# Kernel tuning notes

Measured on AMD Instinct MI355X. Metric: run time of the kernel, lower is better.

Reference implementation:

```python
import jax, jax.numpy as jnp
import numpy as np

T_STEPS, B, I, H = 512, 64, 128, 256
LAST_K, RSIZE = 16, 32


def _xavier(key, shape):
    fan_out, fan_in = shape[0], shape[-1]
    std = (2.0 / (fan_in + fan_out)) ** 0.5
    return (std * jax.random.normal(key, shape)).astype(jnp.float32)


def setup_inputs() -> dict:
    key = jax.random.key(0)
    ks = jax.random.split(key, 8)
    inp = {"x": jax.random.normal(ks[0], (T_STEPS, B, I), dtype=jnp.float32)}
    for n, k in zip(["Wf", "Wi", "Wo", "Wg"], ks[1:5]):
        inp[n + "_w"] = _xavier(k, (H, H + I))
        inp[n + "_b"] = jnp.zeros((H,), jnp.float32)
    inp["Ua_w"] = _xavier(ks[5], (H, H))
    inp["Va_w"] = _xavier(ks[6], (H, H))
    inp["v"] = _xavier(ks[7], (1, H))
    return inp


def _forward(x, Wf_w, Wf_b, Wi_w, Wi_b, Wo_w, Wo_b, Wg_w, Wg_b, Ua_w, Va_w, v):
    T = x.shape[0]
    vv = v[0]  # [H]
    neg_inf = jnp.float32(-jnp.inf)

    def lstm(st, ct, xt):
        inp = jnp.concatenate([st, xt], axis=1)  # [B, H+I], order (hidden, input) as in torch cat((st, x), 1)
        ft = jax.nn.sigmoid(inp @ Wf_w.T + Wf_b)
        it = jax.nn.sigmoid(inp @ Wi_w.T + Wi_b)
        ot = jax.nn.sigmoid(inp @ Wo_w.T + Wo_b)
        gt = jnp.tanh(inp @ Wg_w.T + Wg_b)
        ct = ft * ct + it * gt
        return ot * jnp.tanh(ct), ct

    # ---- step 0 (reset path): st = zero hidden, no attention ----
    st0 = jnp.zeros((B, H), jnp.float32)
    h0, ct0 = lstm(st0, jnp.zeros((B, H), jnp.float32), x[0])
    mem0 = jnp.zeros((LAST_K, B, H), jnp.float32).at[-1].set(h0)  # ring of last_k hiddens (zeros = not yet filled)
    carry0 = (st0, ct0, mem0,
              jnp.zeros((RSIZE, B, H), jnp.float32),   # long_mem buckets
              jnp.full((RSIZE, B), neg_inf),            # long_mask (-inf = empty bucket)
              jnp.zeros((T, B), jnp.float32),           # long_scores (detached accumulator)
              jnp.zeros((B, RSIZE), jnp.float32),       # buck_scores
              jnp.zeros((B,), jnp.int32))               # per-sample bucket fill count

    def body(carry, tx):
        st, ct, mem, long_mem, long_mask, long_scores, buck, fill = carry
        t, xt = tx
        slots = jnp.arange(LAST_K)
        short_valid = slots >= (LAST_K - t)  # slot j holds h_{t-LAST_K+j}; valid iff time >= 0
        # ---- additive attention over short memory + long-term buckets ----
        q = st @ Va_w.T                              # [B,H]
        Uahs = mem @ Ua_w.T                          # [LAST_K,B,H]
        long_uas = long_mem @ Ua_w.T                 # [RSIZE,B,H]
        es = jnp.einsum('kbh,h->kb', jnp.tanh(q[None] + Uahs), vv)
        es = jnp.where(short_valid[:, None], es, neg_inf)
        es_long = jnp.einsum('rbh,h->rb', jnp.tanh(q[None] + long_uas), vv) + long_mask
        alphas = jax.nn.softmax(jnp.concatenate([es, es_long], 0), axis=0)  # [LAST_K+RSIZE,B]
        # accumulate detached attention mass onto absolute-time scores
        det_a = jax.lax.stop_gradient(alphas[:LAST_K])
        times = jnp.clip(t - LAST_K + slots, 0, T - 1)
        long_scores = long_scores.at[times].add(jnp.where(short_valid[:, None], det_a, 0.0))
        comb = jnp.concatenate([mem, long_mem], 0)   # [LAST_K+RSIZE,B,H]
        ct_att = jnp.einsum('nb,nbh->bh', alphas, comb)
        st = 0.5 * (mem[-1] + ct_att)                # comb_hs[-1-rsize] == previous hidden
        # ---- LSTM gating ----
        hidden, ct = lstm(st, ct, xt)
        # ---- bucket insert / argmin-replace (active once t >= LAST_K) ----
        cand = mem[0]                                # h_{t-LAST_K} == memory[0]
        cand_score = jax.lax.stop_gradient(
            jax.lax.dynamic_index_in_dim(long_scores, jnp.clip(t - LAST_K, 0, T - 1), 0, keepdims=False))  # [B]
        minp = jnp.argmin(buck, axis=1)              # [B], first-min like torch.argmin
        min_val = jnp.take_along_axis(buck, minp[:, None], axis=1)[:, 0]
        full = fill >= RSIZE
        addpos = jnp.where(full, minp, fill)
        do_upd = (t >= LAST_K) & (jnp.logical_not(full) | (cand_score > min_val))
        onehot = (jnp.arange(RSIZE)[None, :] == addpos[:, None]) & do_upd[:, None]  # [B,RSIZE]
        sel = onehot.T                               # [RSIZE,B]
        long_mem = jnp.where(sel[:, :, None], cand[None], long_mem)
        long_mask = jnp.where(sel, 0.0, long_mask)
        buck = jnp.where(onehot, cand_score[:, None], buck)
        fill = fill + (do_upd & jnp.logical_not(full)).astype(jnp.int32)
        # ---- push hidden into short-memory ring ----
        mem = jnp.concatenate([mem[1:], hidden[None]], 0)
        return (st, ct, mem, long_mem, long_mask, long_scores, buck, fill), hidden

    ts = jnp.arange(1, T)
    _, hs = jax.lax.scan(jax.checkpoint(body), carry0, (ts, x[1:]))
    return jnp.concatenate([h0[None], hs], 0)  # [T,B,H]


def reference(x, Wf_w, Wf_b, Wi_w, Wi_b, Wo_w, Wo_b, Wg_w, Wg_b, Ua_w, Va_w, v):
    return _forward(x, Wf_w, Wf_b, Wi_w, Wi_b, Wo_w, Wo_b, Wg_w, Wg_b, Ua_w, Va_w, v)
```

## Files before the change

kernel.cpp:

```cpp
#include <hip/hip_runtime.h>
#include <hip/hip_fp16.h>

#define T_STEPS 512
#define NB      64
#define NI      128
#define NH      256
#define LK      16
#define RS      32
#define NS      (LK + RS)

#define WP_OFF   0
#define VAP8_OFF 786432
#define UAP8_OFF 917504
#define GX_OFF   5242880
#define WS_NEED  (GX_OFF + (size_t)T_STEPS * NB * NH * 8)

typedef _Float16 half2v __attribute__((ext_vector_type(2)));

__device__ __forceinline__ float hdot(unsigned int w, unsigned int s, float c) {
    return __builtin_amdgcn_fdot2(__builtin_bit_cast(half2v, w),
                                  __builtin_bit_cast(half2v, s), c, false);
}

__device__ __forceinline__ float fsig(float x) {
    return __builtin_amdgcn_rcpf(1.0f + __expf(-x));
}
__device__ __forceinline__ float ftanh(float x) {
    x = fminf(15.0f, fmaxf(-15.0f, x));
    float e = __expf(2.0f * x);
    return (e - 1.0f) * __builtin_amdgcn_rcpf(e + 1.0f);
}

__global__ void prep_weights(const float* __restrict__ Wf, const float* __restrict__ Wi,
                             const float* __restrict__ Wo, const float* __restrict__ Wg,
                             const float* __restrict__ Ua, const float* __restrict__ Va,
                             unsigned char* __restrict__ ws) {
    int e = blockIdx.x * 256 + threadIdx.x;
    if (e < 49152) {
        int h = e & 255, k2 = e >> 8, k = 2 * k2;
        uint4 w; __half2 t;
        t = __floats2half2_rn(Wf[h * 384 + k], Wf[h * 384 + k + 1]); w.x = *(unsigned int*)&t;
        t = __floats2half2_rn(Wi[h * 384 + k], Wi[h * 384 + k + 1]); w.y = *(unsigned int*)&t;
        t = __floats2half2_rn(Wo[h * 384 + k], Wo[h * 384 + k + 1]); w.z = *(unsigned int*)&t;
        t = __floats2half2_rn(Wg[h * 384 + k], Wg[h * 384 + k + 1]); w.w = *(unsigned int*)&t;
        ((uint4*)(ws + WP_OFF))[e] = w;
    } else {
        int e2 = e - 49152;
        const float* S = (e2 < 8192) ? Va : Ua;
        int e3 = e2 & 8191;
        int h = e3 & 255, j = e3 >> 8, k = 8 * j;
        uint4 w; __half2 t;
        t = __floats2half2_rn(S[h * 256 + k + 0], S[h * 256 + k + 1]); w.x = *(unsigned int*)&t;
        t = __floats2half2_rn(S[h * 256 + k + 2], S[h * 256 + k + 3]); w.y = *(unsigned int*)&t;
        t = __floats2half2_rn(S[h * 256 + k + 4], S[h * 256 + k + 5]); w.z = *(unsigned int*)&t;
        t = __floats2half2_rn(S[h * 256 + k + 6], S[h * 256 + k + 7]); w.w = *(unsigned int*)&t;
        ((uint4*)(ws + VAP8_OFF))[e2] = w;
    }
}

__global__ __launch_bounds__(256) void gx_gemm(const float* __restrict__ x,
                                               unsigned char* __restrict__ ws) {
    const int t = blockIdx.x, bg = blockIdx.y, tid = threadIdx.x;
    const uint4* __restrict__ WP = (const uint4*)(ws + WP_OFF);
    uint2* __restrict__ GX = (uint2*)(ws + GX_OFF);
    __shared__ float s_xx[16 * 128];
    const float* xb = x + ((size_t)t * NB + bg * 16) * NI;
#pragma unroll
    for (int r = 0; r < 8; ++r) s_xx[tid + 256 * r] = xb[tid + 256 * r];
    __syncthreads();
    const int h = tid;
    float acc[16][4];
#pragma unroll
    for (int bb = 0; bb < 16; ++bb) { acc[bb][0] = acc[bb][1] = acc[bb][2] = acc[bb][3] = 0.f; }
    for (int k2 = 128; k2 < 192; ++k2) {
        uint4 w = WP[k2 * NH + h];
        float2 wf = __half22float2(*(const __half2*)&w.x);
        float2 wi = __half22float2(*(const __half2*)&w.y);
        float2 wo = __half22float2(*(const __half2*)&w.z);
        float2 wg = __half22float2(*(const __half2*)&w.w);
        int kk = 2 * k2 - 256;
#pragma unroll
        for (int bb = 0; bb < 16; ++bb) {
            float2 xv = *(const float2*)(s_xx + bb * 128 + kk);
            acc[bb][0] += wf.x * xv.x + wf.y * xv.y;
            acc[bb][1] += wi.x * xv.x + wi.y * xv.y;
            acc[bb][2] += wo.x * xv.x + wo.y * xv.y;
            acc[bb][3] += wg.x * xv.x + wg.y * xv.y;
        }
    }
#pragma unroll
    for (int bb = 0; bb < 16; ++bb) {
        __half2 p0 = __floats2half2_rn(acc[bb][0], acc[bb][1]);
        __half2 p1 = __floats2half2_rn(acc[bb][2], acc[bb][3]);
        uint2 u; u.x = *(unsigned int*)&p0; u.y = *(unsigned int*)&p1;
        GX[((size_t)t * NB + bg * 16 + bb) * NH + h] = u;
    }
}

template <int USE_GX>
__global__ __launch_bounds__(1024, 1) void rel_lstm(
    const float* __restrict__ x,
    const float* __restrict__ bf_g, const float* __restrict__ bi_g,
    const float* __restrict__ bo_g, const float* __restrict__ bg_g,
    const float* __restrict__ vv_g,
    unsigned char* __restrict__ ws, float* __restrict__ out) {
    const int tid = threadIdx.x;
    const int b   = blockIdx.x;
    const int wv  = tid >> 6;
    const int ln  = tid & 63;
    const int h16 = (wv << 4) | (ln & 15);
    const int kc  = ln >> 4;

    const uint4* __restrict__ WP   = (const uint4*)(ws + WP_OFF);
    const uint4* __restrict__ VaP8 = (const uint4*)(ws + VAP8_OFF);
    const uint4* __restrict__ UaP8 = (const uint4*)(ws + UAP8_OFF);
    const uint2* __restrict__ GX   = (const uint2*)(ws + GX_OFF);

    __shared__ __align__(16) _Float16 s_in_h[NH + NI];
    __shared__ __align__(16) _Float16 s_hid_h[NH];
    __shared__ __align__(16) float s_q[NH];
    __shared__ __align__(16) float s_v[NH];
    __shared__ __align__(16) float s_mem[LK][NH];
    __shared__ __align__(16) float s_memua[LK][NH + 8];
    __shared__ __align__(16) float s_lraw[RS * NH];
    __shared__ __align__(16) float s_lua[RS * NH];
    __shared__ float s_es[NS];
    __shared__ float s_scores[T_STEPS];
    __shared__ float s_mask[RS], s_buck[RS];
    __shared__ float s_minv;
    __shared__ int s_minp, s_fill, s_upd, s_pos;

    for (int i = tid; i < LK * NH; i += 1024) ((float*)s_mem)[i] = 0.f;
    for (int i = tid; i < LK * (NH + 8); i += 1024) ((float*)s_memua)[i] = 0.f;
    for (int i = tid; i < RS * NH; i += 1024) { s_lraw[i] = 0.f; s_lua[i] = 0.f; }
    if (tid < T_STEPS) s_scores[tid] = 0.f;
    if (tid < NH) s_v[tid] = vv_g[tid];
    if (tid < (NH + NI) / 2) ((unsigned int*)s_in_h)[tid] = 0u;
    if (tid < RS) { s_mask[tid] = -1e30f; s_buck[tid] = 0.f; }
    if (tid == 0) { s_fill = 0; s_upd = 0; s_pos = 0; s_minv = 0.f; s_minp = 0; }
    float bfv = 0.f, biv = 0.f, bov = 0.f, bgv = 0.f;
    if (kc == 0) { bfv = bf_g[h16]; biv = bi_g[h16]; bov = bo_g[h16]; bgv = bg_g[h16]; }
    if (!USE_GX && tid < 64) {
        float2 xv = ((const float2*)(x + (size_t)b * NI))[tid];
        __half2 hx = __floats2half2_rn(xv.x, xv.y);
        ((unsigned int*)s_in_h)[NH / 2 + tid] = *(unsigned int*)&hx;
    }
    float ct = 0.f;
    int base = 0;
    __syncthreads();

    for (int t = 0; t < T_STEPS; ++t) {
        float evA = 0.f, evB = 0.f;
        uint2 gx = {0u, 0u};
        if (USE_GX && kc == 0) gx = GX[((size_t)t * NB + b) * NH + h16];
        if (t > 0) {
            {
                const uint4* P   = (wv < 8) ? VaP8 : UaP8;
                const uint4* SRC = (wv < 8) ? (const uint4*)s_in_h : (const uint4*)s_hid_h;
                const int hh = ((wv & 7) << 5) | (ln & 31);
                const int ch = ln >> 5;
                float acc = 0.f;
#pragma unroll
                for (int jj = 0; jj < 16; ++jj) {
                    int j = (ch << 4) | jj;
                    uint4 w = P[(j << 8) + hh];
                    uint4 s = SRC[j];
                    acc = hdot(w.x, s.x, acc);
                    acc = hdot(w.y, s.y, acc);
                    acc = hdot(w.z, s.z, acc);
                    acc = hdot(w.w, s.w, acc);
                }
                acc += __shfl_xor(acc, 32, 64);
                if (ch == 0) {
                    if (wv < 8) s_q[hh] = acc;
                    else        s_memua[(base + LK - 1) & (LK - 1)][hh] = acc;
                }
                if (kc == 1) {
                    int p0 = base & (LK - 1);
                    evA = s_mem[p0][h16];
                    evB = s_memua[p0][h16];
                }
                if (!USE_GX && tid < 64) {
                    float2 xv = ((const float2*)(x + ((size_t)t * NB + b) * NI))[tid];
                    __half2 hx = __floats2half2_rn(xv.x, xv.y);
                    ((unsigned int*)s_in_h)[NH / 2 + tid] = *(unsigned int*)&hx;
                }
            }
            __syncthreads();
            if (tid < 768) {
                const int row = tid >> 4, l = tid & 15;
                bool skip;
                const float* ua;
                if (row < LK) { skip = row < LK - t; ua = s_memua[(base + row) & (LK - 1)]; }
                else          { skip = s_mask[row - LK] < -1e29f; ua = s_lua + (row - LK) * NH; }
                float esv = -1e30f;
                if (!skip) {
                    float p = 0.f;
#pragma unroll
                    for (int jj = 0; jj < 4; ++jj) {
                        int hh = (l << 2) + (jj << 6);
                        float4 q4 = *(const float4*)(s_q + hh);
                        float4 v4 = *(const float4*)(s_v + hh);
                        float4 u4 = *(const float4*)(ua + hh);
                        p += v4.x * ftanh(q4.x + u4.x);
                        p += v4.y * ftanh(q4.y + u4.y);
                        p += v4.z * ftanh(q4.z + u4.z);
                        p += v4.w * ftanh(q4.w + u4.w);
                    }
                    p += __shfl_xor(p, 1, 16);
                    p += __shfl_xor(p, 2, 16);
                    p += __shfl_xor(p, 4, 16);
                    p += __shfl_xor(p, 8, 16);
                    esv = p;
                }
                if (l == 0) s_es[row] = esv;
            } else if (tid >= 960 && tid < 992) {
                int l = tid - 960;
                float v = s_buck[l]; int idx = l;
#pragma unroll
                for (int off = 1; off < 32; off <<= 1) {
                    float v2 = __shfl_xor(v, off, 32);
                    int  i2 = __shfl_xor(idx, off, 32);
                    if (v2 < v || (v2 == v && i2 < idx)) { v = v2; idx = i2; }
                }
                if (l == 0) { s_minv = v; s_minp = idx; }
            }
            __syncthreads();
            {
                float e = (ln < NS) ? s_es[ln] : -1e30f;
                float m = e;
#pragma unroll
                for (int off = 32; off; off >>= 1) m = fmaxf(m, __shfl_xor(m, off, 64));
                float a = (ln < NS) ? __expf(e - m) : 0.f;
                float ssum = a;
#pragma unroll
                for (int off = 32; off; off >>= 1) ssum += __shfl_xor(ssum, off, 64);
                float al = a * __builtin_amdgcn_rcpf(ssum);
                if (wv == 0) {
                    float cs = 0.f;
                    if (ln < LK) {
                        int time = t - LK + ln;
                        if (time >= 0) {
                            float ns = s_scores[time] + al;
                            s_scores[time] = ns;
                            cs = ns;
                        }
                    }
                    if (ln == 0) {
                        int upd = 0, pos = 0;
                        if (t >= LK) {
                            int fill = s_fill;
                            bool full = fill >= RS;
                            upd = (!full) || (cs > s_minv);
                            pos = full ? s_minp : fill;
                            if (upd) { s_mask[pos] = 0.f; s_buck[pos] = cs; if (!full) s_fill = fill + 1; }
                        }
                        s_upd = upd; s_pos = pos;
                    }
                }
                float catt = 0.f;
                const int n0 = kc * 12;
#pragma unroll
                for (int n = n0; n < n0 + 12; ++n) {
                    float a2 = __shfl(al, n);
                    if (n < LK) catt += a2 * s_mem[(base + n) & (LK - 1)][h16];
                    else if (a2 != 0.f) catt += a2 * s_lraw[(n - LK) * NH + h16];
                }
                catt += __shfl_xor(catt, 16, 64);
                catt += __shfl_xor(catt, 32, 64);
                if (kc == 0) {
                    float stv = 0.5f * (s_mem[(base + LK - 1) & (LK - 1)][h16] + catt);
                    s_in_h[h16] = (_Float16)stv;
                }
            }
            __syncthreads();
        }
        {
            constexpr int KP = USE_GX ? 32 : 48;
            const unsigned int* S2 = (const unsigned int*)s_in_h;
            float af = 0.f, ai = 0.f, ao = 0.f, ag = 0.f;
            const int lo = kc * KP;
#pragma unroll 8
            for (int k2 = lo; k2 < lo + KP; ++k2) {
                uint4 w = WP[(k2 << 8) + h16];
                unsigned int s2 = S2[k2];
                af = hdot(w.x, s2, af);
                ai = hdot(w.y, s2, ai);
                ao = hdot(w.z, s2, ao);
                ag = hdot(w.w, s2, ag);
            }
            af += __shfl_xor(af, 16, 64); af += __shfl_xor(af, 32, 64);
            ai += __shfl_xor(ai, 16, 64); ai += __shfl_xor(ai, 32, 64);
            ao += __shfl_xor(ao, 16, 64); ao += __shfl_xor(ao, 32, 64);
            ag += __shfl_xor(ag, 16, 64); ag += __shfl_xor(ag, 32, 64);
            if (kc == 0) {
                float pf = af + bfv, pi = ai + biv, po = ao + bov, pg = ag + bgv;
                if (USE_GX) {
                    float2 fi = __half22float2(*(const __half2*)&gx.x);
                    float2 og = __half22float2(*(const __half2*)&gx.y);
                    pf += fi.x; pi += fi.y; po += og.x; pg += og.y;
                }
                float f  = fsig(pf);
                float ii = fsig(pi);
                float o  = fsig(po);
                float g  = ftanh(pg);
                ct = f * ct + ii * g;
                float hid = o * ftanh(ct);
                out[((size_t)t * NB + b) * NH + h16] = hid;
                s_mem[base & (LK - 1)][h16] = hid;
                s_hid_h[h16] = (_Float16)hid;
            } else if (kc == 1 && s_upd) {
                s_lraw[s_pos * NH + h16] = evA;
                s_lua[s_pos * NH + h16]  = evB;
            }
        }
        base++;
        __syncthreads();
    }
}

extern "C" void kernel_launch(void* const* d_in, const int* in_sizes, int n_in,
                              void* d_out, int out_size, void* d_ws, size_t ws_size,
                              hipStream_t stream) {
    const float* x  = (const float*)d_in[0];
    const float* Wf = (const float*)d_in[1];
    const float* bf = (const float*)d_in[2];
    const float* Wi = (const float*)d_in[3];
    const float* bi = (const float*)d_in[4];
    const float* Wo = (const float*)d_in[5];
    const float* bo = (const float*)d_in[6];
    const float* Wg = (const float*)d_in[7];
    const float* bg = (const float*)d_in[8];
    const float* Ua = (const float*)d_in[9];
    const float* Va = (const float*)d_in[10];
    const float* vv = (const float*)d_in[11];
    unsigned char* ws = (unsigned char*)d_ws;
    float* out = (float*)d_out;

    prep_weights<<<256, 256, 0, stream>>>(Wf, Wi, Wo, Wg, Ua, Va, ws);
    if (ws_size >= WS_NEED) {
        gx_gemm<<<dim3(T_STEPS, 4), 256, 0, stream>>>(x, ws);
        rel_lstm<1><<<NB, 1024, 0, stream>>>(x, bf, bi, bo, bg, vv, ws, out);
    } else {
        rel_lstm<0><<<NB, 1024, 0, stream>>>(x, bf, bi, bo, bg, vv, ws, out);
    }
}
```

Baseline: 6.094 ms.

## Precompute per-hidden gate and Va projections in ring buffers, linearly combine by attention

Adds a new recurrent kernel that exploits linearity: instead of building the attended state and then running the gate GEMV and Va GEMV on it, it projects each new hidden state once through W_h (all four gates) and Va, stores those fp16 projections in shared-memory rings alongside the long-memory buckets, and forms the next step's gate preactivations and query as attention-weighted sums of stored projections. This moves the per-step dependent GEMVs off the critical path after the softmax, leaving a cheap 48-term combination. The Ua projection is moved to after the hidden update. It adds extra fp16 rounding of projections and a large shared-memory footprint. The fallback kernel is simplified to a non-templated version.

```diff
diff --git a/kernel.cpp b/kernel.cpp
--- a/kernel.cpp
+++ b/kernel.cpp
@@ -97,8 +97,239 @@
     }
 }
 
-template <int USE_GX>
-__global__ __launch_bounds__(1024, 1) void rel_lstm(
+__global__ __launch_bounds__(1024, 1) void rel_lstm_lin(
+    const float* __restrict__ bf_g, const float* __restrict__ bi_g,
+    const float* __restrict__ bo_g, const float* __restrict__ bg_g,
+    const float* __restrict__ vv_g,
+    unsigned char* __restrict__ ws, float* __restrict__ out) {
+    const int tid = threadIdx.x;
+    const int b   = blockIdx.x;
+    const int wv  = tid >> 6;
+    const int ln  = tid & 63;
+
+    const uint4* __restrict__ WP   = (const uint4*)(ws + WP_OFF);
+    const uint4* __restrict__ VaP8 = (const uint4*)(ws + VAP8_OFF);
+    const uint4* __restrict__ UaP8 = (const uint4*)(ws + UAP8_OFF);
+    const uint2* __restrict__ GX   = (const uint2*)(ws + GX_OFF);
+
+    __shared__ __align__(16) _Float16 WG_ring[48][1024];
+    __shared__ __align__(16) _Float16 Va_ring[48][256];
+    __shared__ __align__(16) _Float16 Ua_ring[48][264];
+    __shared__ __align__(16) float s_gp[1024];
+    __shared__ __align__(16) _Float16 s_hid_h[NH];
+    __shared__ __align__(16) float s_q[NH];
+    __shared__ __align__(16) float s_v[NH];
+    __shared__ float s_al[NS];
+    __shared__ float s_scores[T_STEPS];
+    __shared__ float s_buck[RS];
+    __shared__ int s_fill, s_upd, s_pos;
+
+    unsigned int* WG32 = (unsigned int*)&WG_ring[0][0];
+    unsigned int* VA32 = (unsigned int*)&Va_ring[0][0];
+    unsigned int* UA32 = (unsigned int*)&Ua_ring[0][0];
+
+    for (int i = tid; i < 48 * 512; i += 1024) WG32[i] = 0u;
+    for (int i = tid; i < 48 * 128; i += 1024) VA32[i] = 0u;
+    for (int i = tid; i < 48 * 132; i += 1024) UA32[i] = 0u;
+    if (tid < T_STEPS) s_scores[tid] = 0.f;
+    if (tid < NH) { s_v[tid] = vv_g[tid]; s_q[tid] = 0.f; }
+    if (tid < 128) ((unsigned int*)s_hid_h)[tid] = 0u;
+    if (tid < NS) s_al[tid] = 0.f;
+    if (tid < RS) s_buck[tid] = 0.f;
+    if (tid == 0) { s_fill = 0; s_upd = 0; s_pos = 0; }
+    float bfv = 0.f, biv = 0.f, bov = 0.f, bgv = 0.f;
+    if (tid < NH) { bfv = bf_g[tid]; biv = bi_g[tid]; bov = bo_g[tid]; bgv = bg_g[tid]; }
+    float ct = 0.f;
+    int base = 0;
+    __syncthreads();
+
+    for (int t = 0; t < T_STEPS; ++t) {
+        uint2 gx = {0u, 0u};
+        if (tid < NH) gx = GX[((size_t)t * NB + b) * NH + tid];
+        unsigned int evW = 0u, evV = 0u, evU = 0u;
+        if (t > 0) {
+            const int nslot = (base + LK - 1) & (LK - 1);
+            if (wv < 8) {
+                const int h = (wv << 5) | (ln & 31);
+                const int kh = ln >> 5;
+                const unsigned int* H2 = (const unsigned int*)s_hid_h;
+                float af = 0.f, ai = 0.f, ao = 0.f, ag = 0.f;
+#pragma unroll 8
+                for (int k2 = kh * 64; k2 < kh * 64 + 64; ++k2) {
+                    uint4 w = WP[(k2 << 8) + h];
+                    unsigned int s2 = H2[k2];
+                    af = hdot(w.x, s2, af); ai = hdot(w.y, s2, ai);
+                    ao = hdot(w.z, s2, ao); ag = hdot(w.w, s2, ag);
+                }
+                af += __shfl_xor(af, 32); ai += __shfl_xor(ai, 32);
+                ao += __shfl_xor(ao, 32); ag += __shfl_xor(ag, 32);
+                if (kh == 0) {
+                    _Float16* row = WG_ring[nslot];
+                    row[h]       = (_Float16)af;
+                    row[256 + h] = (_Float16)ai;
+                    row[512 + h] = (_Float16)ao;
+                    row[768 + h] = (_Float16)ag;
+                }
+            } else if (wv < 12) {
+                const int h = ((wv - 8) << 6) | ln;
+                const uint4* H4 = (const uint4*)s_hid_h;
+                float acc = 0.f;
+#pragma unroll 8
+                for (int j = 0; j < 32; ++j) {
+                    uint4 w = VaP8[(j << 8) + h];
+                    uint4 s = H4[j];
+                    acc = hdot(w.x, s.x, acc); acc = hdot(w.y, s.y, acc);
+                    acc = hdot(w.z, s.z, acc); acc = hdot(w.w, s.w, acc);
+                }
+                Va_ring[nslot][h] = (_Float16)acc;
+            } else if (wv == 12) {
+                const int s4 = ln & 3;
+                float e[3];
+#pragma unroll
+                for (int m = 0; m < 3; ++m) {
+                    int row = m * 16 + (ln >> 2);
+                    bool skip; const _Float16* ua;
+                    if (row < LK) { skip = row < LK - t; ua = Ua_ring[(base + row) & (LK - 1)]; }
+                    else          { skip = (row - LK) >= s_fill; ua = Ua_ring[row]; }
+                    float p = -1e30f;
+                    if (!skip) {
+                        p = 0.f;
+#pragma unroll
+                        for (int q = 0; q < 16; ++q) {
+                            int h0 = s4 * 4 + q * 16;
+                            float4 q4 = *(const float4*)(s_q + h0);
+                            float4 v4 = *(const float4*)(s_v + h0);
+                            uint2 uh = *(const uint2*)(ua + h0);
+                            float2 a0 = __half22float2(*(const __half2*)&uh.x);
+                            float2 a1 = __half22float2(*(const __half2*)&uh.y);
+                            p += v4.x * ftanh(q4.x + a0.x) + v4.y * ftanh(q4.y + a0.y)
+                               + v4.z * ftanh(q4.z + a1.x) + v4.w * ftanh(q4.w + a1.y);
+                        }
+                        p += __shfl_xor(p, 1, 4);
+                        p += __shfl_xor(p, 2, 4);
+                    }
+                    e[m] = p;
+                }
+                int src = (ln & 15) << 2;
+                float f0 = __shfl(e[0], src), f1 = __shfl(e[1], src), f2 = __shfl(e[2], src);
+                float ee = (ln < 16) ? f0 : (ln < 32) ? f1 : (ln < 48) ? f2 : -1e30f;
+                float mm = ee;
+#pragma unroll
+                for (int off = 32; off; off >>= 1) mm = fmaxf(mm, __shfl_xor(mm, off));
+                float a = (ln < NS) ? __expf(ee - mm) : 0.f;
+                float ssum = a;
+#pragma unroll
+                for (int off = 32; off; off >>= 1) ssum += __shfl_xor(ssum, off);
+                float al = a * __builtin_amdgcn_rcpf(ssum);
+                if (ln < NS) s_al[ln] = al;
+                float bv = (ln < RS) ? s_buck[ln] : 1e30f;
+                int   bi2 = (ln < RS) ? ln : 999;
+#pragma unroll
+                for (int off = 1; off < 32; off <<= 1) {
+                    float v2 = __shfl_xor(bv, off, 32);
+                    int   i2 = __shfl_xor(bi2, off, 32);
+                    if (v2 < bv || (v2 == bv && i2 < bi2)) { bv = v2; bi2 = i2; }
+                }
+                float cs = 0.f;
+                if (ln < LK) {
+                    int time = t - LK + ln;
+                    if (time >= 0) { float ns = s_scores[time] + al; s_scores[time] = ns; cs = ns; }
+                }
+                if (ln == 0) {
+                    int upd = 0, pos = 0;
+                    if (t >= LK) {
+                        int fill = s_fill;
+                        bool full = fill >= RS;
+                        upd = (!full) || (cs > bv);
+                        pos = full ? bi2 : fill;
+                        if (upd) { s_buck[pos] = cs; if (!full) s_fill = fill + 1; }
+                    }
+                    s_upd = upd; s_pos = pos;
+                }
+            }
+            __syncthreads();
+            {
+                const int eslot = base & (LK - 1);
+                if (tid < 512) {
+                    float a0 = 0.f, a1 = 0.f;
+#pragma unroll
+                    for (int n = 0; n < NS; ++n) {
+                        int slot = (n < LK) ? ((base + n) & (LK - 1)) : n;
+                        float c = s_al[n] + ((n == LK - 1) ? 1.0f : 0.0f);
+                        unsigned int u = WG32[slot * 512 + tid];
+                        float2 f = __half22float2(*(const __half2*)&u);
+                        a0 += c * f.x; a1 += c * f.y;
+                    }
+                    s_gp[2 * tid]     = 0.5f * a0;
+                    s_gp[2 * tid + 1] = 0.5f * a1;
+                    evW = WG32[eslot * 512 + tid];
+                } else if (tid < 640) {
+                    const int d = tid - 512;
+                    float a0 = 0.f, a1 = 0.f;
+#pragma unroll
+                    for (int n = 0; n < NS; ++n) {
+                        int slot = (n < LK) ? ((base + n) & (LK - 1)) : n;
+                        float c = s_al[n] + ((n == LK - 1) ? 1.0f : 0.0f);
+                        unsigned int u = VA32[slot * 128 + d];
+                        float2 f = __half22float2(*(const __half2*)&u);
+                        a0 += c * f.x; a1 += c * f.y;
+                    }
+                    s_q[2 * d]     = 0.5f * a0;
+                    s_q[2 * d + 1] = 0.5f * a1;
+                    evV = VA32[eslot * 128 + d];
+                } else if (tid < 768) {
+                    evU = UA32[eslot * 132 + (tid - 640)];
+                }
+            }
+            __syncthreads();
+        }
+        if (tid < NH) {
+            float pf = bfv, pi = biv, po = bov, pg = bgv;
+            if (t > 0) {
+                pf += s_gp[tid];       pi += s_gp[256 + tid];
+                po += s_gp[512 + tid]; pg += s_gp[768 + tid];
+            }
+            float2 fi = __half22float2(*(const __half2*)&gx.x);
+            float2 og = __half22float2(*(const __half2*)&gx.y);
+            pf += fi.x; pi += fi.y; po += og.x; pg += og.y;
+            float f  = fsig(pf);
+            float ii = fsig(pi);
+            float o  = fsig(po);
+            float g  = ftanh(pg);
+            ct = f * ct + ii * g;
+            float hid = o * ftanh(ct);
+            out[((size_t)t * NB + b) * NH + tid] = hid;
+            s_hid_h[tid] = (_Float16)hid;
+        }
+        if (t > 0 && s_upd) {
+            const int lrow = LK + s_pos;
+            if (tid < 512)      WG32[lrow * 512 + tid] = evW;
+            else if (tid < 640) VA32[lrow * 128 + (tid - 512)] = evV;
+            else if (tid < 768) UA32[lrow * 132 + (tid - 640)] = evU;
+        }
+        __syncthreads();
+        {
+            const int h = (wv << 4) | (ln & 15);
+            const int kc = ln >> 4;
+            const uint4* H4 = (const uint4*)s_hid_h;
+            float acc = 0.f;
+#pragma unroll
+            for (int j = 0; j < 8; ++j) {
+                int jj = kc * 8 + j;
+                uint4 w = UaP8[(jj << 8) + h];
+                uint4 s = H4[jj];
+                acc = hdot(w.x, s.x, acc); acc = hdot(w.y, s.y, acc);
+                acc = hdot(w.z, s.z, acc); acc = hdot(w.w, s.w, acc);
+            }
+            acc += __shfl_xor(acc, 16); acc += __shfl_xor(acc, 32);
+            if (kc == 0) Ua_ring[base & (LK - 1)][h] = (_Float16)acc;
+        }
+        base++;
+        __syncthreads();
+    }
+}
+
+__global__ __launch_bounds__(1024, 1) void rel_lstm_mono(
     const float* __restrict__ x,
     const float* __restrict__ bf_g, const float* __restrict__ bi_g,
     const float* __restrict__ bo_g, const float* __restrict__ bg_g,
@@ -114,7 +345,6 @@
     const uint4* __restrict__ WP   = (const uint4*)(ws + WP_OFF);
     const uint4* __restrict__ VaP8 = (const uint4*)(ws + VAP8_OFF);
     const uint4* __restrict__ UaP8 = (const uint4*)(ws + UAP8_OFF);
-    const uint2* __restrict__ GX   = (const uint2*)(ws + GX_OFF);
 
     __shared__ __align__(16) _Float16 s_in_h[NH + NI];
     __shared__ __align__(16) _Float16 s_hid_h[NH];
@@ -124,7 +354,7 @@
     __shared__ __align__(16) float s_memua[LK][NH + 8];
     __shared__ __align__(16) float s_lraw[RS * NH];
     __shared__ __align__(16) float s_lua[RS * NH];
-    __shared__ float s_es[NS];
+    __shared__ float s_es[NS], s_al[NS];
     __shared__ float s_scores[T_STEPS];
     __shared__ float s_mask[RS], s_buck[RS];
     __shared__ float s_minv;
@@ -140,7 +370,7 @@
     if (tid == 0) { s_fill = 0; s_upd = 0; s_pos = 0; s_minv = 0.f; s_minp = 0; }
     float bfv = 0.f, biv = 0.f, bov = 0.f, bgv = 0.f;
     if (kc == 0) { bfv = bf_g[h16]; biv = bi_g[h16]; bov = bo_g[h16]; bgv = bg_g[h16]; }
-    if (!USE_GX && tid < 64) {
+    if (tid < 64) {
         float2 xv = ((const float2*)(x + (size_t)b * NI))[tid];
         __half2 hx = __floats2half2_rn(xv.x, xv.y);
         ((unsigned int*)s_in_h)[NH / 2 + tid] = *(unsigned int*)&hx;
@@ -151,8 +381,6 @@
 
     for (int t = 0; t < T_STEPS; ++t) {
         float evA = 0.f, evB = 0.f;
-        uint2 gx = {0u, 0u};
-        if (USE_GX && kc == 0) gx = GX[((size_t)t * NB + b) * NH + h16];
         if (t > 0) {
             {
                 const uint4* P   = (wv < 8) ? VaP8 : UaP8;
@@ -180,7 +408,7 @@
                     evA = s_mem[p0][h16];
                     evB = s_memua[p0][h16];
                 }
-                if (!USE_GX && tid < 64) {
+                if (tid < 64) {
                     float2 xv = ((const float2*)(x + ((size_t)t * NB + b) * NI))[tid];
                     __half2 hx = __floats2half2_rn(xv.x, xv.y);
                     ((unsigned int*)s_in_h)[NH / 2 + tid] = *(unsigned int*)&hx;
@@ -226,45 +454,47 @@
                 if (l == 0) { s_minv = v; s_minp = idx; }
             }
             __syncthreads();
-            {
-                float e = (ln < NS) ? s_es[ln] : -1e30f;
+            if (tid < 64) {
+                float e = (tid < NS) ? s_es[tid] : -1e30f;
                 float m = e;
 #pragma unroll
                 for (int off = 32; off; off >>= 1) m = fmaxf(m, __shfl_xor(m, off, 64));
-                float a = (ln < NS) ? __expf(e - m) : 0.f;
+                float a = (tid < NS) ? __expf(e - m) : 0.f;
                 float ssum = a;
 #pragma unroll
                 for (int off = 32; off; off >>= 1) ssum += __shfl_xor(ssum, off, 64);
                 float al = a * __builtin_amdgcn_rcpf(ssum);
-                if (wv == 0) {
-                    float cs = 0.f;
-                    if (ln < LK) {
-                        int time = t - LK + ln;
-                        if (time >= 0) {
-                            float ns = s_scores[time] + al;
-                            s_scores[time] = ns;
-                            cs = ns;
-                        }
-                    }
-                    if (ln == 0) {
-                        int upd = 0, pos = 0;
-                        if (t >= LK) {
-                            int fill = s_fill;
-                            bool full = fill >= RS;
-                            upd = (!full) || (cs > s_minv);
-                            pos = full ? s_minp : fill;
-                            if (upd) { s_mask[pos] = 0.f; s_buck[pos] = cs; if (!full) s_fill = fill + 1; }
-                        }
-                        s_upd = upd; s_pos = pos;
-                    }
-                }
+                if (tid < NS) s_al[tid] = al;
+                float cs = 0.f;
+                if (tid < LK) {
+                    int time = t - LK + tid;
+                    if (time >= 0) {
+                        float ns = s_scores[time] + al;
+                        s_scores[time] = ns;
+                        cs = ns;
+                    }
+                }
+                if (tid == 0) {
+                    int upd = 0, pos = 0;
+                    if (t >= LK) {
+                        int fill = s_fill;
+                        bool full = fill >= RS;
+                        upd = (!full) || (cs > s_minv);
+                        pos = full ? s_minp : fill;
+                        if (upd) { s_mask[pos] = 0.f; s_buck[pos] = cs; if (!full) s_fill = fill + 1; }
+                    }
+                    s_upd = upd; s_pos = pos;
+                }
+            }
+            __syncthreads();
+            {
                 float catt = 0.f;
                 const int n0 = kc * 12;
 #pragma unroll
                 for (int n = n0; n < n0 + 12; ++n) {
-                    float a2 = __shfl(al, n);
-                    if (n < LK) catt += a2 * s_mem[(base + n) & (LK - 1)][h16];
-                    else if (a2 != 0.f) catt += a2 * s_lraw[(n - LK) * NH + h16];
+                    float a = s_al[n];
+                    if (n < LK) catt += a * s_mem[(base + n) & (LK - 1)][h16];
+                    else if (a != 0.f) catt += a * s_lraw[(n - LK) * NH + h16];
                 }
                 catt += __shfl_xor(catt, 16, 64);
                 catt += __shfl_xor(catt, 32, 64);
@@ -276,12 +506,11 @@
             __syncthreads();
         }
         {
-            constexpr int KP = USE_GX ? 32 : 48;
             const unsigned int* S2 = (const unsigned int*)s_in_h;
             float af = 0.f, ai = 0.f, ao = 0.f, ag = 0.f;
-            const int lo = kc * KP;
+            const int lo = kc * 48;
 #pragma unroll 8
-            for (int k2 = lo; k2 < lo + KP; ++k2) {
+            for (int k2 = lo; k2 < lo + 48; ++k2) {
                 uint4 w = WP[(k2 << 8) + h16];
                 unsigned int s2 = S2[k2];
                 af = hdot(w.x, s2, af);
@@ -294,16 +523,10 @@
             ao += __shfl_xor(ao, 16, 64); ao += __shfl_xor(ao, 32, 64);
             ag += __shfl_xor(ag, 16, 64); ag += __shfl_xor(ag, 32, 64);
             if (kc == 0) {
-                float pf = af + bfv, pi = ai + biv, po = ao + bov, pg = ag + bgv;
-                if (USE_GX) {
-                    float2 fi = __half22float2(*(const __half2*)&gx.x);
-                    float2 og = __half22float2(*(const __half2*)&gx.y);
-                    pf += fi.x; pi += fi.y; po += og.x; pg += og.y;
-                }
-                float f  = fsig(pf);
-                float ii = fsig(pi);
-                float o  = fsig(po);
-                float g  = ftanh(pg);
+                float f  = fsig(af + bfv);
+                float ii = fsig(ai + biv);
+                float o  = fsig(ao + bov);
+                float g  = ftanh(ag + bgv);
                 ct = f * ct + ii * g;
                 float hid = o * ftanh(ct);
                 out[((size_t)t * NB + b) * NH + h16] = hid;
@@ -340,8 +563,8 @@
     prep_weights<<<256, 256, 0, stream>>>(Wf, Wi, Wo, Wg, Ua, Va, ws);
     if (ws_size >= WS_NEED) {
         gx_gemm<<<dim3(T_STEPS, 4), 256, 0, stream>>>(x, ws);
-        rel_lstm<1><<<NB, 1024, 0, stream>>>(x, bf, bi, bo, bg, vv, ws, out);
+        rel_lstm_lin<<<NB, 1024, 0, stream>>>(bf, bi, bo, bg, vv, ws, out);
     } else {
-        rel_lstm<0><<<NB, 1024, 0, stream>>>(x, bf, bi, bo, bg, vv, ws, out);
-    }
-}
+        rel_lstm_mono<<<NB, 1024, 0, stream>>>(x, bf, bi, bo, bg, vv, ws, out);
+    }
+}
```

Result: no change. 6.096 ms (+0.0%).
